# Kernel tuning notes

Hardware: AMD Instinct MI355X
Metric: run time of the kernel (lower is better)

## Reference

```python
import jax, jax.numpy as jnp
import numpy as np

L, N, C, OPL = 20, 512, 10, 13        # levels, nodes/level, conditions/node, condition op length
HID, MID = 512, 256                   # hidden_dim, hid_dim
OP_DIM, EX_DIM, SAMP_DIM = 15, 108, 1000
EPS = 1e-5


def _lstm_cell(x, h, c, wih, whh, bih, bhh):
    gates = x @ wih.T + h @ whh.T + bih + bhh
    i, f, g, o = jnp.split(gates, 4, axis=-1)  # torch gate order i,f,g,o
    c = jax.nn.sigmoid(f) * c + jax.nn.sigmoid(i) * jnp.tanh(g)
    h = jax.nn.sigmoid(o) * jnp.tanh(c)
    return h, c


def _batchnorm(x, g, b):  # training-mode BatchNorm1d (biased batch stats)
    m = x.mean(0)
    v = x.var(0)
    return (x - m) / jnp.sqrt(v + EPS) * g + b


def setup_inputs() -> dict:
    key = jax.random.key(0)
    ks = iter(jax.random.split(key, 48))
    rn = lambda shp, s=1.0: jax.random.normal(next(ks), shp, jnp.float32) * s
    ru = lambda shp: jax.random.uniform(next(ks), shp, jnp.float32)
    w = lambda shp: rn(shp, 0.05)
    inp = {
        'operators': ru((L, N, OP_DIM)),
        'extra_infos': rn((L, N, EX_DIM)),
        'condition1s': rn((L, N, C, OPL)),
        'condition2s': rn((L, N, C, OPL)),
        'samples': ru((L, N, SAMP_DIM)),
        'condition_masks': jnp.ones((L, N, 1), jnp.float32),
        'mapping': jax.random.randint(next(ks), (L, 2, N), 0, N + 1),
        # lstm1 (condition encoder)
        'w_ih1': w((4 * HID, OPL)), 'w_hh1': w((4 * HID, HID)),
        'b_ih1': w((4 * HID,)), 'b_hh1': w((4 * HID,)),
        # mlps feeding the tree lstm
        'sample_w': w((MID, SAMP_DIM)), 'sample_b': w((MID,)),
        'cond_w': w((MID, HID)), 'cond_b': w((MID,)),
        'bn1_g': jnp.ones((MID,), jnp.float32), 'bn1_b': jnp.zeros((MID,), jnp.float32),
        # lstm2 (tree aggregation)
        'w_ih2': w((4 * HID, OP_DIM + EX_DIM + 2 * MID)), 'w_hh2': w((4 * HID, HID)),
        'b_ih2': w((4 * HID,)), 'b_hh2': w((4 * HID,)),
        'bn2_g': jnp.ones((HID,), jnp.float32), 'bn2_b': jnp.zeros((HID,), jnp.float32),
        # task heads
        't1_w2': w((MID, HID)), 't1_b2': w((MID,)),
        't2_w2': w((MID, HID)), 't2_b2': w((MID,)),
        'bn3_g': jnp.ones((MID,), jnp.float32), 'bn3_b': jnp.zeros((MID,), jnp.float32),
        't1_w3': w((MID, MID)), 't1_b3': w((MID,)),
        't2_w3': w((MID, MID)), 't2_b3': w((MID,)),
        't1_ow': w((1, MID)), 't1_ob': w((1,)),
        't2_ow': w((1, MID)), 't2_ob': w((1,)),
    }
    return inp


def reference(operators, extra_infos, condition1s, condition2s, samples, condition_masks, mapping,
              w_ih1, w_hh1, b_ih1, b_hh1, sample_w, sample_b, cond_w, cond_b, bn1_g, bn1_b,
              w_ih2, w_hh2, b_ih2, b_hh2, bn2_g, bn2_b,
              t1_w2, t1_b2, t2_w2, t2_b2, bn3_g, bn3_b,
              t1_w3, t1_b3, t2_w3, t2_b3, t1_ow, t1_ob, t2_ow, t2_ob):
    Lv, Np = operators.shape[0], operators.shape[1]
    mapping = mapping.astype(jnp.int32)

    # --- condition encoder: lstm1 over each node's predicate sequence ---
    x = condition1s.reshape(Lv * Np, C, OPL)
    h0 = jnp.zeros((Lv * Np, HID), operators.dtype)

    def step1(carry, xt):
        h, c = carry
        h, c = _lstm_cell(xt, h, c, w_ih1, w_hh1, b_ih1, b_hh1)
        return (h, c), None

    (h_last, _), _ = jax.lax.scan(step1, (h0, h0), jnp.swapaxes(x, 0, 1))
    cond = _batchnorm(jax.nn.relu(h_last @ cond_w.T + cond_b), bn1_g, bn1_b)
    cond = cond.reshape(Lv, Np, MID)

    samp = jax.nn.relu(samples @ sample_w.T + sample_b) * condition_masks
    feats = jnp.concatenate([operators, extra_infos, cond, samp], axis=2)  # [L, N, 123+2*MID]

    # --- bottom level: lstm2 single step from zero state ---
    z0 = jnp.zeros((Np, HID), feats.dtype)
    hid, cid = _lstm_cell(feats[Lv - 1], z0, z0, w_ih2, w_hh2, b_ih2, b_hh2)

    # --- bottom-up tree aggregation: gather children states, average, lstm2 step ---
    def level_step(carry, inputs):
        hid, cid = carry
        x_lvl, mapp = inputs  # x_lvl [N, F], mapp [2, N], index 0 == pad (no child)
        pad = jnp.zeros((1, HID), hid.dtype)
        nh = jnp.concatenate([pad, hid], axis=0)  # [N+1, H]
        nc = jnp.concatenate([pad, cid], axis=0)
        h = (nh[mapp[0]] + nh[mapp[1]]) * 0.5
        c = (nc[mapp[0]] + nc[mapp[1]]) * 0.5
        hid, cid = _lstm_cell(x_lvl, h, c, w_ih2, w_hh2, b_ih2, b_hh2)
        return (hid, cid), None

    xs = (feats[Lv - 2::-1], mapping[Lv - 2::-1])
    (hid, cid), _ = jax.lax.scan(level_step, (hid, cid), xs)

    # --- heads (batch_size == Np: all level-0 nodes active for these inputs) ---
    z = _batchnorm(hid, bn2_g, bn2_b)
    t1 = _batchnorm(jax.nn.relu(z @ t1_w2.T + t1_b2), bn3_g, bn3_b)
    t1 = jax.nn.sigmoid(jax.nn.relu(t1 @ t1_w3.T + t1_b3) @ t1_ow.T + t1_ob)
    t2 = _batchnorm(jax.nn.relu(z @ t2_w2.T + t2_b2), bn3_g, bn3_b)
    t2 = jax.nn.sigmoid(jax.nn.relu(t2 @ t2_w3.T + t2_b3) @ t2_ow.T + t2_ob)
    return t1, t2
```

## Files before the change

kernel.cpp:

```cpp
#include <hip/hip_runtime.h>
#include <hip/hip_bf16.h>


typedef __bf16 bf16x8 __attribute__((ext_vector_type(8)));
typedef float f32x4 __attribute__((ext_vector_type(4)));

#define MROWS 10240
#define LDH1  552
#define L1_ROWS 48
#define L1_BLOCKS 214
#define SAMP_BASE 214
#define FEAT_BASE 374
#define FUSED_BLOCKS 414

#define PF_BIAS1   0
#define PF_BIAS2   2048
#define PF_CONDB   4096
#define PF_SAMPB   4352
#define PF_BCAT2   4608
#define PF_B3CAT   5120
#define PF_BN1G    5632
#define PF_BN1B    5888
#define PF_BN2G    6144
#define PF_BN2B    6656
#define PF_BN3G    7168
#define PF_BN3B    7424
#define PF_OW      7680
#define PF_OB      8192
#define PF_TOTAL   8194

__device__ __forceinline__ float fsig(float x) {
  return __builtin_amdgcn_rcpf(1.0f + __expf(-x));
}
__device__ __forceinline__ float ftanh(float x) {
  return fmaf(2.0f, __builtin_amdgcn_rcpf(1.0f + __expf(-2.0f * x)), -1.0f);
}
__device__ __forceinline__ bf16x8 bzero8() {
  bf16x8 z;
#pragma unroll
  for (int i = 0; i < 8; ++i) z[i] = (__bf16)0.0f;
  return z;
}
__device__ __forceinline__ float ld_in(const void* p, long i, int bf) {
  return bf ? (float)((const __bf16*)p)[i] : ((const float*)p)[i];
}

__global__ void detect_kernel(const unsigned* __restrict__ masks, int* __restrict__ flag) {
  if (blockIdx.x == 0 && threadIdx.x == 0)
    *flag = (masks[0] == 0x3F803F80u) ? 1 : 0;
}

__global__ void prep_kernel(const int* __restrict__ flagp,
    const void* w_ih1, const void* w_hh1, const void* b_ih1, const void* b_hh1,
    const void* w_ih2, const void* w_hh2, const void* b_ih2, const void* b_hh2,
    const void* t1_w2, const void* t2_w2, const void* t1_b2, const void* t2_b2,
    const void* cond_w, const void* cond_b, const void* sample_w, const void* sample_b,
    const void* bn1_g, const void* bn1_b, const void* bn2_g, const void* bn2_b,
    const void* bn3_g, const void* bn3_b,
    const void* t1_w3, const void* t1_b3, const void* t2_w3, const void* t2_b3,
    const void* t1_ow, const void* t1_ob, const void* t2_ow, const void* t2_ob,
    const void* masks,
    __bf16* __restrict__ w1s, __bf16* __restrict__ w2s,
    __bf16* __restrict__ wcat2, __bf16* __restrict__ cond_w_bf,
    __bf16* __restrict__ sample_w_bf, __bf16* __restrict__ w3cat_bf,
    float* __restrict__ mask_f, float* __restrict__ pf)
{
  const int bf = *flagp;
  const int S1 = 2048 * 544;
  const int S2 = 2048 * 1152;
  const int S3 = 512 * 512;
  const int S4 = 256 * 512;
  const int S5 = 256 * 1000;
  const int S6 = 512 * 256;
  const int S7 = 10240;
  const int total = S1 + S2 + S3 + S4 + S5 + S6 + S7 + PF_TOTAL;
  for (int idx = blockIdx.x * blockDim.x + threadIdx.x; idx < total;
       idx += gridDim.x * blockDim.x) {
    int i = idx;
    if (i < S1) {
      int e = i & 7, l = (i >> 3) & 63, g = (i >> 9) & 3;
      int grp = i >> 11;
      int kk = grp % 17, cgt = grp / 17;
      int colq = l & 15, quad = l >> 4;
      int row = g * 512 + cgt * 16 + colq;
      int k = kk * 32 + quad * 8 + e;
      float v = (k < 512) ? ld_in(w_hh1, (long)row * 512 + k, bf)
              : (k < 525) ? ld_in(w_ih1, (long)row * 13 + (k - 512), bf) : 0.0f;
      w1s[i] = (__bf16)v;
      continue;
    }
    i -= S1;
    if (i < S2) {
      int e = i & 7, l = (i >> 3) & 63, g = (i >> 9) & 3;
      int grp = i >> 11;
      int kk = grp % 36, jt = grp / 36;
      int colq = l & 15, quad = l >> 4;
      int row = g * 512 + jt * 16 + colq;
      int k = kk * 32 + quad * 8 + e;
      float v = (k < 635) ? ld_in(w_ih2, (long)row * 635 + k, bf)
              : (k < 640) ? 0.0f : ld_in(w_hh2, (long)row * 512 + (k - 640), bf);
      w2s[i] = (__bf16)v;
      continue;
    }
    i -= S2;
    if (i < S3) {
      int r = i >> 9, k = i & 511;
      wcat2[i] = (__bf16)((r < 256) ? ld_in(t1_w2, r * 512 + k, bf)
                                    : ld_in(t2_w2, (r - 256) * 512 + k, bf));
      continue;
    }
    i -= S3;
    if (i < S4) { cond_w_bf[i] = (__bf16)ld_in(cond_w, i, bf); continue; }
    i -= S4;
    if (i < S5) { sample_w_bf[i] = (__bf16)ld_in(sample_w, i, bf); continue; }
    i -= S5;
    if (i < S6) {
      int r = i >> 8, k = i & 255;
      w3cat_bf[i] = (__bf16)((r < 256) ? ld_in(t1_w3, r * 256 + k, bf)
                                       : ld_in(t2_w3, (r - 256) * 256 + k, bf));
      continue;
    }
    i -= S6;
    if (i < S7) { mask_f[i] = ld_in(masks, i, bf); continue; }
    i -= S7;
    {
      int j = i;
      float v;
      if      (j < 2048) v = ld_in(b_ih1, j, bf) + ld_in(b_hh1, j, bf);
      else if (j < 4096) v = ld_in(b_ih2, j - 2048, bf) + ld_in(b_hh2, j - 2048, bf);
      else if (j < 4352) v = ld_in(cond_b, j - 4096, bf);
      else if (j < 4608) v = ld_in(sample_b, j - 4352, bf);
      else if (j < 5120) { int k = j - 4608; v = (k < 256) ? ld_in(t1_b2, k, bf) : ld_in(t2_b2, k - 256, bf); }
      else if (j < 5632) { int k = j - 5120; v = (k < 256) ? ld_in(t1_b3, k, bf) : ld_in(t2_b3, k - 256, bf); }
      else if (j < 5888) v = ld_in(bn1_g, j - 5632, bf);
      else if (j < 6144) v = ld_in(bn1_b, j - 5888, bf);
      else if (j < 6656) v = ld_in(bn2_g, j - 6144, bf);
      else if (j < 7168) v = ld_in(bn2_b, j - 6656, bf);
      else if (j < 7424) v = ld_in(bn3_g, j - 7168, bf);
      else if (j < 7680) v = ld_in(bn3_b, j - 7424, bf);
      else if (j < 8192) { int k = j - 7680; v = (k < 256) ? ld_in(t1_ow, k, bf) : ld_in(t2_ow, k - 256, bf); }
      else v = (j == 8192) ? ld_in(t1_ob, 0, bf) : ld_in(t2_ob, 0, bf);
      pf[j] = v;
    }
  }
}

__global__ void conv_samples_kernel(const int* __restrict__ flagp,
                                    const void* __restrict__ samples,
                                    __bf16* __restrict__ dst)
{
  const int bf = *flagp;
  if (bf) return;
  for (long i = blockIdx.x * blockDim.x + threadIdx.x; i < 10240000L;
       i += (long)gridDim.x * blockDim.x)
    dst[i] = (__bf16)ld_in(samples, i, bf);
}

__global__ __launch_bounds__(1024, 4) void fused1_kernel(
    const int* __restrict__ flagp,
    const void* __restrict__ cond1,
    const __bf16* __restrict__ w1s,
    const float*  __restrict__ bias,
    __bf16* __restrict__ h_out,
    const void* __restrict__ samples_raw,
    const __bf16* __restrict__ samp_bf,
    const __bf16* __restrict__ sample_w_bf,
    const float* __restrict__ sampb,
    __bf16* __restrict__ samp_out,
    const float* __restrict__ mask,
    const void* __restrict__ ops,
    const void* __restrict__ extra,
    __bf16* __restrict__ Astage)
{
  const int bf = *flagp;
  const int tid = threadIdx.x;

  if (blockIdx.x < L1_BLOCKS) {
    __shared__ __attribute__((aligned(16))) __bf16 hbuf[2][L1_ROWS * LDH1];
    const int wave = tid >> 6;
    const int lane = tid & 63;
    const int colq = lane & 15;
    const int quad = lane >> 4;
    const int r0   = blockIdx.x * L1_ROWS;

    {
      bf16x8 z8 = bzero8();
      for (int i = tid * 8; i < 2 * L1_ROWS * LDH1; i += 1024 * 8)
        *(bf16x8*)&hbuf[0][i] = z8;
    }
    __syncthreads();
    if (tid < L1_ROWS * 8) {
      int row = tid >> 3, jj = tid & 7;
      int gr = r0 + row;
      if (gr < MROWS) {
        long base = (long)gr * 130;
        hbuf[0][row * LDH1 + 512 + jj] = (__bf16)ld_in(cond1, base + jj, bf);
        if (jj < 5) hbuf[0][row * LDH1 + 520 + jj] = (__bf16)ld_in(cond1, base + 8 + jj, bf);
      }
    }
    __syncthreads();

    float c_reg[2][3][4];
#pragma unroll
    for (int a = 0; a < 2; ++a)
#pragma unroll
      for (int b = 0; b < 3; ++b)
#pragma unroll
        for (int r = 0; r < 4; ++r) c_reg[a][b][r] = 0.0f;

    const int jbase = wave * 32;

    float bI[2], bF[2], bG[2], bO[2];
#pragma unroll
    for (int cg = 0; cg < 2; ++cg) {
      const int j = jbase + cg * 16 + colq;
      bI[cg] = bias[j];
      bF[cg] = bias[512 + j];
      bG[cg] = bias[1024 + j];
      bO[cg] = bias[1536 + j];
    }

#pragma unroll 1
    for (int t = 0; t < 10; ++t) {
      const __bf16* hcur = hbuf[t & 1];
      __bf16* hnxt = hbuf[(t + 1) & 1];
#pragma unroll
      for (int cg = 0; cg < 2; ++cg) {
        const int jc = jbase + cg * 16;
        f32x4 acc[3][4];
#pragma unroll
        for (int a = 0; a < 3; ++a)
#pragma unroll
          for (int g = 0; g < 4; ++g)
#pragma unroll
            for (int r = 0; r < 4; ++r) acc[a][g][r] = 0.0f;

        const __bf16* wp = w1s + ((size_t)(wave * 2 + cg) * 17 * 4 * 512) + (lane << 3);
#pragma unroll 1
        for (int kk = 0; kk < 17; ++kk) {
          const int kof = (kk << 5) + (quad << 3);
          bf16x8 af[3];
#pragma unroll
          for (int rt = 0; rt < 3; ++rt)
            af[rt] = *(const bf16x8*)&hcur[(rt * 16 + colq) * LDH1 + kof];
          bf16x8 bfr[4];
#pragma unroll
          for (int g = 0; g < 4; ++g)
            bfr[g] = *(const bf16x8*)&wp[(kk * 4 + g) << 9];
#pragma unroll
          for (int g = 0; g < 4; ++g)
#pragma unroll
            for (int rt = 0; rt < 3; ++rt)
              acc[rt][g] = __builtin_amdgcn_mfma_f32_16x16x32_bf16(af[rt], bfr[g], acc[rt][g], 0, 0, 0);
        }
#pragma unroll
        for (int rt = 0; rt < 3; ++rt)
#pragma unroll
          for (int r = 0; r < 4; ++r) {
            float c = fsig(acc[rt][1][r] + bF[cg]) * c_reg[cg][rt][r]
                    + fsig(acc[rt][0][r] + bI[cg]) * ftanh(acc[rt][2][r] + bG[cg]);
            c_reg[cg][rt][r] = c;
            float h = fsig(acc[rt][3][r] + bO[cg]) * ftanh(c);
            hnxt[(rt * 16 + quad * 4 + r) * LDH1 + jc + colq] = (__bf16)h;
          }
      }
      if (t < 9 && tid < L1_ROWS * 8) {
        int row = tid >> 3, jj = tid & 7;
        int gr = r0 + row;
        if (gr < MROWS) {
          long base = ((long)gr * 10 + (t + 1)) * 13;
          hnxt[row * LDH1 + 512 + jj] = (__bf16)ld_in(cond1, base + jj, bf);
          if (jj < 5) hnxt[row * LDH1 + 520 + jj] = (__bf16)ld_in(cond1, base + 8 + jj, bf);
        }
      }
      __syncthreads();
    }

    for (int i = tid; i < L1_ROWS * 64; i += 1024) {
      int row = i >> 6;
      int cb  = (i & 63) << 3;
      *(bf16x8*)&h_out[(size_t)(r0 + row) * 512 + cb] = *(const bf16x8*)&hbuf[0][row * LDH1 + cb];
    }
    return;
  }

  if (blockIdx.x < FEAT_BASE) {
    const __bf16* A = bf ? (const __bf16*)samples_raw : samp_bf;
    const int vb   = (blockIdx.x - SAMP_BASE) * 4 + (tid >> 8);
    const int bx   = vb & 3;
    const int by   = vb >> 2;
    const int t    = tid & 255;
    const int wave = t >> 6;
    const int lane = t & 63;
    const int colq = lane & 15;
    const int quad = lane >> 4;
    const int m0 = by * 64 + (wave >> 1) * 32;
    const int n0 = bx * 64 + (wave & 1) * 32;
    const int K = 1000;

    f32x4 acc[2][2];
#pragma unroll
    for (int a = 0; a < 2; ++a)
#pragma unroll
      for (int b = 0; b < 2; ++b)
#pragma unroll
        for (int r = 0; r < 4; ++r) acc[a][b][r] = 0.0f;

    for (int kk = 0; kk < 32; ++kk) {
      const int kof = (kk << 5) + (quad << 3);
      bf16x8 a0, a1, b0, b1;
      if (kof < K) {
        a0 = *(const bf16x8*)&A[(size_t)(m0 + colq) * 1000 + kof];
        a1 = *(const bf16x8*)&A[(size_t)(m0 + 16 + colq) * 1000 + kof];
        b0 = *(const bf16x8*)&sample_w_bf[(size_t)(n0 + colq) * 1000 + kof];
        b1 = *(const bf16x8*)&sample_w_bf[(size_t)(n0 + 16 + colq) * 1000 + kof];
      } else {
        a0 = bzero8(); a1 = a0; b0 = a0; b1 = a0;
      }
      acc[0][0] = __builtin_amdgcn_mfma_f32_16x16x32_bf16(a0, b0, acc[0][0], 0, 0, 0);
      acc[0][1] = __builtin_amdgcn_mfma_f32_16x16x32_bf16(a0, b1, acc[0][1], 0, 0, 0);
      acc[1][0] = __builtin_amdgcn_mfma_f32_16x16x32_bf16(a1, b0, acc[1][0], 0, 0, 0);
      acc[1][1] = __builtin_amdgcn_mfma_f32_16x16x32_bf16(a1, b1, acc[1][1], 0, 0, 0);
    }
#pragma unroll
    for (int ai = 0; ai < 2; ++ai)
#pragma unroll
      for (int bi = 0; bi < 2; ++bi) {
        const int col = n0 + bi * 16 + colq;
        const float bv = sampb[col];
#pragma unroll
        for (int r = 0; r < 4; ++r) {
          const int row = m0 + ai * 16 + quad * 4 + r;
          float v = fmaxf(acc[ai][bi][r] + bv, 0.0f) * mask[row];
          samp_out[(size_t)row * 640 + col] = (__bf16)v;
        }
      }
    return;
  }

  for (int idx = (blockIdx.x - FEAT_BASE) * 1024 + tid; idx < 10240 * 128;
       idx += 40 * 1024) {
    int m = idx >> 7, c = idx & 127;
    float v; int col;
    if (c < 15)       { v = ld_in(ops, (long)m * 15 + c, bf);            col = c; }
    else if (c < 123) { v = ld_in(extra, (long)m * 108 + (c - 15), bf);  col = c; }
    else              { v = 0.0f;                                        col = 512 + c; }
    Astage[(size_t)m * 640 + col] = (__bf16)v;
  }
}

template<int ACT, int OUTBF, int MASKED>
__global__ __launch_bounds__(256, 4) void gemm_kernel(
    const __bf16* __restrict__ A, int lda,
    const __bf16* __restrict__ W, int ldw,
    const float* __restrict__ bias,
    float* __restrict__ outf, __bf16* __restrict__ outb, int ldc,
    const float* __restrict__ mask, int K)
{
  const int tid  = threadIdx.x;
  const int wave = tid >> 6;
  const int lane = tid & 63;
  const int colq = lane & 15;
  const int quad = lane >> 4;
  const int m0 = blockIdx.y * 64 + (wave >> 1) * 32;
  const int n0 = blockIdx.x * 64 + (wave & 1) * 32;

  f32x4 acc[2][2];
#pragma unroll
  for (int a = 0; a < 2; ++a)
#pragma unroll
    for (int b = 0; b < 2; ++b)
#pragma unroll
      for (int r = 0; r < 4; ++r) acc[a][b][r] = 0.0f;

  const int nk = (K + 31) >> 5;
  for (int kk = 0; kk < nk; ++kk) {
    const int kof = (kk << 5) + (quad << 3);
    bf16x8 a0, a1, b0, b1;
    if (kof < K) {
      a0 = *(const bf16x8*)&A[(size_t)(m0 + colq) * lda + kof];
      a1 = *(const bf16x8*)&A[(size_t)(m0 + 16 + colq) * lda + kof];
      b0 = *(const bf16x8*)&W[(size_t)(n0 + colq) * ldw + kof];
      b1 = *(const bf16x8*)&W[(size_t)(n0 + 16 + colq) * ldw + kof];
    } else {
      a0 = bzero8(); a1 = a0; b0 = a0; b1 = a0;
    }
    acc[0][0] = __builtin_amdgcn_mfma_f32_16x16x32_bf16(a0, b0, acc[0][0], 0, 0, 0);
    acc[0][1] = __builtin_amdgcn_mfma_f32_16x16x32_bf16(a0, b1, acc[0][1], 0, 0, 0);
    acc[1][0] = __builtin_amdgcn_mfma_f32_16x16x32_bf16(a1, b0, acc[1][0], 0, 0, 0);
    acc[1][1] = __builtin_amdgcn_mfma_f32_16x16x32_bf16(a1, b1, acc[1][1], 0, 0, 0);
  }
#pragma unroll
  for (int ai = 0; ai < 2; ++ai)
#pragma unroll
    for (int bi = 0; bi < 2; ++bi) {
      const int col = n0 + bi * 16 + colq;
      const float bv = bias[col];
#pragma unroll
      for (int r = 0; r < 4; ++r) {
        const int row = m0 + ai * 16 + quad * 4 + r;
        float v = acc[ai][bi][r] + bv;
        if (ACT) v = fmaxf(v, 0.0f);
        if (MASKED) v *= mask[row];
        if (OUTBF) outb[(size_t)row * ldc + col] = (__bf16)v;
        else       outf[(size_t)row * ldc + col] = v;
      }
    }
}

__global__ __launch_bounds__(1024, 4) void treelvl_kernel(
    const __bf16* __restrict__ Alvl,
    const __bf16* __restrict__ w2s,
    const float* __restrict__ bias,
    const int* __restrict__ mapping,
    const __bf16* __restrict__ h_src, const float* __restrict__ c_src,
    __bf16* __restrict__ h_dst, float* __restrict__ c_dst,
    float* __restrict__ h_f32, int first, int last)
{
  __shared__ float red[3][16 * 256];
  const int tid  = threadIdx.x;
  const int wave = tid >> 6;
  const int lane = tid & 63;
  const int colq = lane & 15;
  const int quad = lane >> 4;
  const int wv   = wave & 3;
  const int kq   = wave >> 2;
  const int jt = blockIdx.x;
  const int mt = blockIdx.y;
  const int rowA = mt * 64 + wv * 16 + colq;

  const __bf16* wbase = w2s + (size_t)jt * 36 * 4 * 512 + (lane << 3);

  f32x4 acc[4];
#pragma unroll
  for (int g = 0; g < 4; ++g)
#pragma unroll
    for (int r = 0; r < 4; ++r) acc[g][r] = 0.0f;

  if (kq < 2) {
    const __bf16* arow = Alvl + (size_t)rowA * 640;
    const int kb = kq * 10;
#pragma unroll 2
    for (int ki = 0; ki < 10; ++ki) {
      const int kk = kb + ki;
      const int kof = (kk << 5) + (quad << 3);
      bf16x8 afr = *(const bf16x8*)&arow[kof];
      bf16x8 b0 = *(const bf16x8*)&wbase[(kk * 4 + 0) << 9];
      bf16x8 b1 = *(const bf16x8*)&wbase[(kk * 4 + 1) << 9];
      bf16x8 b2 = *(const bf16x8*)&wbase[(kk * 4 + 2) << 9];
      bf16x8 b3 = *(const bf16x8*)&wbase[(kk * 4 + 3) << 9];
      acc[0] = __builtin_amdgcn_mfma_f32_16x16x32_bf16(afr, b0, acc[0], 0, 0, 0);
      acc[1] = __builtin_amdgcn_mfma_f32_16x16x32_bf16(afr, b1, acc[1], 0, 0, 0);
      acc[2] = __builtin_amdgcn_mfma_f32_16x16x32_bf16(afr, b2, acc[2], 0, 0, 0);
      acc[3] = __builtin_amdgcn_mfma_f32_16x16x32_bf16(afr, b3, acc[3], 0, 0, 0);
    }
  } else {
    int i0 = 0, i1 = 0;
    if (!first) { i0 = mapping[rowA]; i1 = mapping[512 + rowA]; }
    const float s0 = (i0 > 0) ? 0.5f : 0.0f;
    const float s1 = (i1 > 0) ? 0.5f : 0.0f;
    const __bf16* h0p = h_src + (size_t)((i0 > 0 ? i0 : 1) - 1) * 512;
    const __bf16* h1p = h_src + (size_t)((i1 > 0 ? i1 : 1) - 1) * 512;
    const int kb = 20 + (kq - 2) * 8;
#pragma unroll 2
    for (int ki = 0; ki < 8; ++ki) {
      const int kk = kb + ki;
      const int kh = ((kk - 20) << 5) + (quad << 3);
      bf16x8 v0 = *(const bf16x8*)&h0p[kh];
      bf16x8 v1 = *(const bf16x8*)&h1p[kh];
      bf16x8 afr;
#pragma unroll
      for (int e = 0; e < 8; ++e)
        afr[e] = (__bf16)((float)v0[e] * s0 + (float)v1[e] * s1);
      bf16x8 b0 = *(const bf16x8*)&wbase[(kk * 4 + 0) << 9];
      bf16x8 b1 = *(const bf16x8*)&wbase[(kk * 4 + 1) << 9];
      bf16x8 b2 = *(const bf16x8*)&wbase[(kk * 4 + 2) << 9];
      bf16x8 b3 = *(const bf16x8*)&wbase[(kk * 4 + 3) << 9];
      acc[0] = __builtin_amdgcn_mfma_f32_16x16x32_bf16(afr, b0, acc[0], 0, 0, 0);
      acc[1] = __builtin_amdgcn_mfma_f32_16x16x32_bf16(afr, b1, acc[1], 0, 0, 0);
      acc[2] = __builtin_amdgcn_mfma_f32_16x16x32_bf16(afr, b2, acc[2], 0, 0, 0);
      acc[3] = __builtin_amdgcn_mfma_f32_16x16x32_bf16(afr, b3, acc[3], 0, 0, 0);
    }
  }

  if (kq > 0) {
    float* rp = red[kq - 1];
    const int base = wv * 64 + lane;
#pragma unroll
    for (int g = 0; g < 4; ++g)
#pragma unroll
      for (int r = 0; r < 4; ++r)
        rp[(g * 4 + r) * 256 + base] = acc[g][r];
  }
  __syncthreads();
  if (kq != 0) return;

  {
    const int base = wv * 64 + lane;
#pragma unroll
    for (int s = 0; s < 3; ++s) {
      const float* rp = red[s];
#pragma unroll
      for (int g = 0; g < 4; ++g)
#pragma unroll
        for (int r = 0; r < 4; ++r)
          acc[g][r] += rp[(g * 4 + r) * 256 + base];
    }
  }

  const int j = jt * 16 + colq;
  const float bi  = bias[j];
  const float bff = bias[512 + j];
  const float bg  = bias[1024 + j];
  const float bo  = bias[1536 + j];
#pragma unroll
  for (int r = 0; r < 4; ++r) {
    const int mrow = mt * 64 + wv * 16 + quad * 4 + r;
    float ci = 0.0f;
    if (!first) {
      int a0 = mapping[mrow], a1 = mapping[512 + mrow];
      if (a0 > 0) ci += c_src[(size_t)(a0 - 1) * 512 + j];
      if (a1 > 0) ci += c_src[(size_t)(a1 - 1) * 512 + j];
      ci *= 0.5f;
    }
    float c = fsig(acc[1][r] + bff) * ci + fsig(acc[0][r] + bi) * ftanh(acc[2][r] + bg);
    float h = fsig(acc[3][r] + bo) * ftanh(c);
    h_dst[(size_t)mrow * 512 + j] = (__bf16)h;
    c_dst[(size_t)mrow * 512 + j] = c;
    if (last) h_f32[(size_t)mrow * 512 + j] = h;
  }
}

__global__ void stats1_kernel(const float* __restrict__ in, int ld, int N,
                              int rows_per_blk, float* __restrict__ partial)
{
  int b = blockIdx.x;
  int r0 = b * rows_per_blk;
  for (int c = threadIdx.x; c < N; c += blockDim.x) {
    float s = 0.0f, sq = 0.0f;
    for (int r = 0; r < rows_per_blk; ++r) {
      float v = in[(size_t)(r0 + r) * ld + c];
      s += v; sq += v * v;
    }
    partial[(size_t)(2 * b) * N + c] = s;
    partial[(size_t)(2 * b + 1) * N + c] = sq;
  }
}

__global__ void stats2_kernel(const float* __restrict__ partial, int nb, int N,
                              float invM, float* __restrict__ stats)
{
  int c = blockIdx.x * blockDim.x + threadIdx.x;
  if (c >= N) return;
  float s = 0.0f, sq = 0.0f;
  for (int b = 0; b < nb; ++b) {
    s  += partial[(size_t)(2 * b) * N + c];
    sq += partial[(size_t)(2 * b + 1) * N + c];
  }
  float mean = s * invM;
  float var  = sq * invM - mean * mean;
  stats[c]     = mean;
  stats[N + c] = rsqrtf(fmaxf(var, 0.0f) + 1e-5f);
}

__global__ void norm_kernel(const float* __restrict__ in, int ldin,
                            const float* __restrict__ stats, int N, int cshift, int gmask,
                            const float* __restrict__ g, const float* __restrict__ b,
                            __bf16* __restrict__ outp, int ldc, int total)
{
  for (int idx = blockIdx.x * blockDim.x + threadIdx.x; idx < total;
       idx += gridDim.x * blockDim.x) {
    int row = idx >> cshift;
    int c = idx & (N - 1);
    float v = (in[(size_t)row * ldin + c] - stats[c]) * stats[N + c];
    int gi = c & gmask;
    v = v * g[gi] + b[gi];
    outp[(size_t)row * ldc + c] = (__bf16)v;
  }
}

__global__ void head_kernel(const int* __restrict__ flagp,
                            const __bf16* __restrict__ tmp3,
                            const float* __restrict__ pf,
                            void* __restrict__ outp)
{
  const int bf = *flagp;
  const int gw   = blockIdx.x * 4 + (threadIdx.x >> 6);
  const int lane = threadIdx.x & 63;
  const int which = gw >> 9;
  const int n     = gw & 511;
  const __bf16* row = tmp3 + (size_t)n * 512 + which * 256;
  const float* ow = pf + PF_OW + which * 256;
  float s = 0.0f;
#pragma unroll
  for (int i = 0; i < 4; ++i) {
    const int k = lane + 64 * i;
    s += (float)row[k] * ow[k];
  }
#pragma unroll
  for (int off = 32; off > 0; off >>= 1)
    s += __shfl_down(s, off);
  if (lane == 0) {
    float v = fsig(s + pf[PF_OB + which]);
    if (bf) ((__bf16*)outp)[gw] = (__bf16)v;
    else    ((float*)outp)[gw]  = v;
  }
}

extern "C" void kernel_launch(void* const* d_in, const int* in_sizes, int n_in,
                              void* d_out, int out_size, void* d_ws, size_t ws_size,
                              hipStream_t stream) {
  const void* operators       = d_in[0];
  const void* extra_infos     = d_in[1];
  const void* condition1s     = d_in[2];
  const void* samples         = d_in[4];
  const void* condition_masks = d_in[5];
  const int*  mapping         = (const int*)d_in[6];
  (void)in_sizes; (void)n_in; (void)out_size; (void)ws_size;

  char* ws = (char*)d_ws;
  size_t off = 0;
  auto alloc = [&](size_t bytes) -> void* {
    void* p = ws + off;
    off += (bytes + 255) & ~(size_t)255;
    return p;
  };
  int*    flag     = (int*)   alloc(256);
  __bf16* w1s      = (__bf16*)alloc((size_t)2048 * 544 * 2);
  __bf16* w2s      = (__bf16*)alloc((size_t)2048 * 1152 * 2);
  __bf16* wcat2    = (__bf16*)alloc(512 * 512 * 2);
  __bf16* cond_w_bf   = (__bf16*)alloc(256 * 512 * 2);
  __bf16* sample_w_bf = (__bf16*)alloc(256 * 1000 * 2);
  __bf16* w3cat_bf    = (__bf16*)alloc(512 * 256 * 2);
  float*  mask_f   = (float*) alloc(10240 * 4);
  float*  pf       = (float*) alloc(PF_TOTAL * 4);
  __bf16* samp_bf  = (__bf16*)alloc((size_t)10240 * 1000 * 2);
  __bf16* h_last   = (__bf16*)alloc((size_t)10272 * 512 * 2);
  float*  condtmp  = (float*) alloc((size_t)10240 * 256 * 4);
  __bf16* Astage   = (__bf16*)alloc((size_t)20 * 512 * 640 * 2);
  __bf16* hs0      = (__bf16*)alloc(512 * 512 * 2);
  __bf16* hs1      = (__bf16*)alloc(512 * 512 * 2);
  float*  cs0      = (float*) alloc(512 * 512 * 4);
  float*  cs1      = (float*) alloc(512 * 512 * 4);
  float*  h_f32    = (float*) alloc(512 * 512 * 4);
  __bf16* zbuf     = (__bf16*)alloc(512 * 512 * 2);
  float*  tmp1     = (float*) alloc(512 * 512 * 4);
  __bf16* tmp2     = (__bf16*)alloc(512 * 512 * 2);
  __bf16* tmp3     = (__bf16*)alloc(512 * 512 * 2);
  float*  partial  = (float*) alloc(64 * 2 * 512 * 4);
  float*  statsb   = (float*) alloc(2 * 512 * 4);

  detect_kernel<<<1, 64, 0, stream>>>((const unsigned*)condition_masks, flag);
  prep_kernel<<<4096, 256, 0, stream>>>(flag,
      d_in[7], d_in[8], d_in[9], d_in[10],
      d_in[17], d_in[18], d_in[19], d_in[20],
      d_in[23], d_in[25], d_in[24], d_in[26],
      d_in[13], d_in[14], d_in[11], d_in[12],
      d_in[15], d_in[16], d_in[21], d_in[22],
      d_in[27], d_in[28],
      d_in[29], d_in[30], d_in[31], d_in[32],
      d_in[33], d_in[34], d_in[35], d_in[36],
      condition_masks,
      w1s, w2s, wcat2, cond_w_bf, sample_w_bf, w3cat_bf, mask_f, pf);

  conv_samples_kernel<<<4096, 256, 0, stream>>>(flag, samples, samp_bf);

  fused1_kernel<<<FUSED_BLOCKS, 1024, 0, stream>>>(flag,
      condition1s, w1s, pf + PF_BIAS1, h_last,
      samples, samp_bf, sample_w_bf, pf + PF_SAMPB, Astage + 379, mask_f,
      operators, extra_infos, Astage);

  gemm_kernel<1,0,0><<<dim3(4,160), 256, 0, stream>>>(h_last, 512, cond_w_bf, 512,
      pf + PF_CONDB, condtmp, nullptr, 256, nullptr, 512);
  stats1_kernel<<<64, 256, 0, stream>>>(condtmp, 256, 256, 160, partial);
  stats2_kernel<<<1, 256, 0, stream>>>(partial, 64, 256, 1.0f / 10240.0f, statsb);
  norm_kernel<<<2560, 256, 0, stream>>>(condtmp, 256, statsb, 256, 8, 255,
      pf + PF_BN1G, pf + PF_BN1B, Astage + 123, 640, 10240 * 256);

  for (int lvl = 19; lvl >= 0; --lvl) {
    __bf16* hd = (lvl & 1) ? hs1 : hs0;
    float*  cd = (lvl & 1) ? cs1 : cs0;
    const __bf16* hsrc = (lvl & 1) ? hs0 : hs1;
    const float*  csrc = (lvl & 1) ? cs0 : cs1;
    treelvl_kernel<<<dim3(32,8), 1024, 0, stream>>>(
        Astage + (size_t)lvl * 512 * 640, w2s, pf + PF_BIAS2,
        mapping + lvl * 1024, hsrc, csrc, hd, cd, h_f32,
        (lvl == 19) ? 1 : 0, (lvl == 0) ? 1 : 0);
  }

  stats1_kernel<<<8, 256, 0, stream>>>(h_f32, 512, 512, 64, partial);
  stats2_kernel<<<2, 256, 0, stream>>>(partial, 8, 512, 1.0f / 512.0f, statsb);
  norm_kernel<<<256, 256, 0, stream>>>(h_f32, 512, statsb, 512, 9, 511,
      pf + PF_BN2G, pf + PF_BN2B, zbuf, 512, 512 * 512);

  gemm_kernel<1,0,0><<<dim3(8,8), 256, 0, stream>>>(zbuf, 512, wcat2, 512,
      pf + PF_BCAT2, tmp1, nullptr, 512, nullptr, 512);
  stats1_kernel<<<8, 256, 0, stream>>>(tmp1, 512, 512, 64, partial);
  stats2_kernel<<<2, 256, 0, stream>>>(partial, 8, 512, 1.0f / 512.0f, statsb);
  norm_kernel<<<256, 256, 0, stream>>>(tmp1, 512, statsb, 512, 9, 255,
      pf + PF_BN3G, pf + PF_BN3B, tmp2, 512, 512 * 512);

  gemm_kernel<1,1,0><<<dim3(4,8), 256, 0, stream>>>(tmp2, 512, w3cat_bf, 256,
      pf + PF_B3CAT, nullptr, tmp3, 512, nullptr, 256);
  gemm_kernel<1,1,0><<<dim3(4,8), 256, 0, stream>>>(tmp2 + 256, 512, w3cat_bf + 256 * 256, 256,
      pf + PF_B3CAT + 256, nullptr, tmp3 + 256, 512, nullptr, 256);

  head_kernel<<<256, 256, 0, stream>>>(flag, tmp3, pf, d_out);
}
```

Before: 934.6 us.

## Fuse condition MLP GEMM and BN1 partial stats into LSTM1 blocks

After the condition LSTM finishes, each LSTM1 block multiplies its final hidden states, still in shared memory, by cond_w with MFMA, applies bias and ReLU, writes condtmp, and emits per-block column sums and sums of squares. This replaces the separate cond GEMM and stats1 launches and avoids re-reading h_last from global memory. In exchange, stats2 now reduces 214 partials instead of 64, and the LSTM1 blocks take on extra serial work at their tail.

```diff
diff --git a/kernel.cpp b/kernel.cpp
--- a/kernel.cpp
+++ b/kernel.cpp
@@ -170,7 +170,11 @@
     const float* __restrict__ mask,
     const void* __restrict__ ops,
     const void* __restrict__ extra,
-    __bf16* __restrict__ Astage)
+    __bf16* __restrict__ Astage,
+    const __bf16* __restrict__ cond_w_bf,
+    const float* __restrict__ condb,
+    float* __restrict__ condtmp,
+    float* __restrict__ partial)
 {
   const int bf = *flagp;
   const int tid = threadIdx.x;
@@ -280,6 +284,49 @@
       int row = i >> 6;
       int cb  = (i & 63) << 3;
       *(bf16x8*)&h_out[(size_t)(r0 + row) * 512 + cb] = *(const bf16x8*)&hbuf[0][row * LDH1 + cb];
+    }
+
+    {
+      const int ct = wave;
+      f32x4 cacc[3];
+#pragma unroll
+      for (int rt = 0; rt < 3; ++rt)
+#pragma unroll
+        for (int r = 0; r < 4; ++r) cacc[rt][r] = 0.0f;
+
+      const __bf16* wb = cond_w_bf + (size_t)(ct * 16 + colq) * 512;
+#pragma unroll 1
+      for (int kk = 0; kk < 16; ++kk) {
+        const int kof = (kk << 5) + (quad << 3);
+        bf16x8 bfr = *(const bf16x8*)&wb[kof];
+#pragma unroll
+        for (int rt = 0; rt < 3; ++rt) {
+          bf16x8 af = *(const bf16x8*)&hbuf[0][(rt * 16 + colq) * LDH1 + kof];
+          cacc[rt] = __builtin_amdgcn_mfma_f32_16x16x32_bf16(af, bfr, cacc[rt], 0, 0, 0);
+        }
+      }
+      const int col = ct * 16 + colq;
+      const float bv = condb[col];
+      float s1 = 0.0f, s2 = 0.0f;
+#pragma unroll
+      for (int rt = 0; rt < 3; ++rt)
+#pragma unroll
+        for (int r = 0; r < 4; ++r) {
+          const int lrow = rt * 16 + quad * 4 + r;
+          const int grow = r0 + lrow;
+          float v = fmaxf(cacc[rt][r] + bv, 0.0f);
+          if (grow < MROWS) {
+            condtmp[(size_t)grow * 256 + col] = v;
+            s1 += v;
+            s2 += v * v;
+          }
+        }
+      s1 += __shfl_xor(s1, 16); s2 += __shfl_xor(s2, 16);
+      s1 += __shfl_xor(s1, 32); s2 += __shfl_xor(s2, 32);
+      if (quad == 0) {
+        partial[(size_t)(2 * blockIdx.x) * 256 + col]     = s1;
+        partial[(size_t)(2 * blockIdx.x + 1) * 256 + col] = s2;
+      }
     }
     return;
   }
@@ -647,7 +694,7 @@
   float*  tmp1     = (float*) alloc(512 * 512 * 4);
   __bf16* tmp2     = (__bf16*)alloc(512 * 512 * 2);
   __bf16* tmp3     = (__bf16*)alloc(512 * 512 * 2);
-  float*  partial  = (float*) alloc(64 * 2 * 512 * 4);
+  float*  partial  = (float*) alloc((size_t)214 * 2 * 256 * 4 + 8 * 2 * 512 * 4);
   float*  statsb   = (float*) alloc(2 * 512 * 4);
 
   detect_kernel<<<1, 64, 0, stream>>>((const unsigned*)condition_masks, flag);
@@ -668,12 +715,10 @@
   fused1_kernel<<<FUSED_BLOCKS, 1024, 0, stream>>>(flag,
       condition1s, w1s, pf + PF_BIAS1, h_last,
       samples, samp_bf, sample_w_bf, pf + PF_SAMPB, Astage + 379, mask_f,
-      operators, extra_infos, Astage);
-
-  gemm_kernel<1,0,0><<<dim3(4,160), 256, 0, stream>>>(h_last, 512, cond_w_bf, 512,
-      pf + PF_CONDB, condtmp, nullptr, 256, nullptr, 512);
-  stats1_kernel<<<64, 256, 0, stream>>>(condtmp, 256, 256, 160, partial);
-  stats2_kernel<<<1, 256, 0, stream>>>(partial, 64, 256, 1.0f / 10240.0f, statsb);
+      operators, extra_infos, Astage,
+      cond_w_bf, pf + PF_CONDB, condtmp, partial);
+
+  stats2_kernel<<<1, 256, 0, stream>>>(partial, 214, 256, 1.0f / 10240.0f, statsb);
   norm_kernel<<<2560, 256, 0, stream>>>(condtmp, 256, statsb, 256, 8, 255,
       pf + PF_BN1G, pf + PF_BN1B, Astage + 123, 640, 10240 * 256);
 
```

New measurement: 922.0 us. Within noise of the previous version (-1.3%).
